# Performance work log

Hardware: AMD Instinct MI355X
Metric: run time of the kernel (lower is better)

## Reference

```python
import jax, jax.numpy as jnp
import numpy as np

EPS = 1e-7  # keras.backend.epsilon()
ROUTINGS = 3


def squash(s, axis=-1):
    # standard capsule squash: ||s||^2/(1+||s||^2) * s/||s||
    n2 = jnp.sum(jnp.square(s), axis=axis, keepdims=True)
    return s * (n2 / (1.0 + n2)) / jnp.sqrt(n2 + EPS)


def setup_inputs() -> dict:
    key = jax.random.key(0)
    k1, k2 = jax.random.split(key)
    B, I, K = 32, 2048, 8          # batch, input capsules, input capsule dim
    J, D = 32, 16                  # output capsules (num_capsules), dim_capsules
    x = jax.random.normal(k1, (B, I, K), dtype=jnp.float32)
    # add_weight with random_normal_initializer(stddev=0.1), shape [J, I, D, K]
    W = 0.1 * jax.random.normal(k2, (J, I, D, K), dtype=jnp.float32)
    return {"x": x, "W": W}


def reference(x, W):
    # u_ji_hat[b,j,i,d] = sum_k W[j,i,d,k] * x[b,i,k]  (the map_fn batched matmul)
    u_hat = jnp.einsum('jidk,bik->bjid', W, x)  # [B, J, I, D]
    B, J, I, D = u_hat.shape
    b = jnp.zeros((B, J, I), dtype=u_hat.dtype)  # routing logits b_ij
    v = None
    for r in range(ROUTINGS):
        c = jax.nn.softmax(b, axis=1)                 # softmax over output capsules J
        s = jnp.einsum('bji,bjid->bjd', c, u_hat)     # weighted sum over input caps i
        v = squash(s, axis=-1)                        # squash over capsule dim (axis=-2 pre-squeeze)
        if r < ROUTINGS - 1:
            # agreement = u_hat^T v : sum over capsule dim d
            b = b + jnp.einsum('bjid,bjd->bji', u_hat, v)
    return v  # [B, J, D] == tf.squeeze(v_j, [2, 4])
```

## Files before the change

kernel.cpp:

```cpp
#include <hip/hip_runtime.h>
#include <hip/hip_fp16.h>


#define ICAP    2048
#define JD      512
#define S_ELEMS 16384
#define EPSQ    1e-7f
#define NBP     256
#define ICH     8

#if defined(__has_builtin) && __has_builtin(__builtin_amdgcn_rcpf)
#define FAST_RCP(x) __builtin_amdgcn_rcpf(x)
#else
#define FAST_RCP(x) (1.0f / (x))
#endif
#if defined(__has_builtin) && __has_builtin(__builtin_amdgcn_rsqf)
#define FAST_RSQ(x) __builtin_amdgcn_rsqf(x)
#else
#define FAST_RSQ(x) rsqrtf(x)
#endif

__global__ __launch_bounds__(256)
void caps_transpose(const float4* __restrict__ Wv, float4* __restrict__ Wt) {
    __shared__ float4 buf[16 * 66];
    const int i = blockIdx.x;
    const int t = threadIdx.x;
#pragma unroll
    for (int q = 0; q < 4; ++q) {
        const int f = q * 256 + t;
        const int jj = f >> 5, c = f & 31;
        buf[(c & 15) * 66 + 2 * jj + (c >> 4)] =
            Wv[(size_t)jj * 65536 + (size_t)i * 32 + c];
    }
    __syncthreads();
    float4* dst = Wt + (size_t)i * 1024;
#pragma unroll
    for (int q = 0; q < 4; ++q) {
        const int o = q * 256 + t;
        dst[o] = buf[(o >> 6) * 66 + (o & 63)];
    }
}

__global__ __launch_bounds__(512, 1)
void caps_pass(const float4* __restrict__ Wt, const float* __restrict__ x,
               const float* __restrict__ vsum, __half* __restrict__ partials) {
    const int tid  = threadIdx.x;
    const int wave = tid >> 6;
    const int lane = tid & 63;
    const int j    = lane & 31;
    const int dh   = lane >> 5;
    const int i0   = blockIdx.x * ICH;

    float vs[4][8], sacc[4][8];
#pragma unroll
    for (int bb = 0; bb < 4; ++bb) {
        const int b = wave + 8 * bb;
        const float* vp = vsum + b * JD + j * 16 + dh * 8;
        float4 a  = *reinterpret_cast<const float4*>(vp);
        float4 bq = *reinterpret_cast<const float4*>(vp + 4);
        vs[bb][0]=a.x; vs[bb][1]=a.y; vs[bb][2]=a.z; vs[bb][3]=a.w;
        vs[bb][4]=bq.x; vs[bb][5]=bq.y; vs[bb][6]=bq.z; vs[bb][7]=bq.w;
#pragma unroll
        for (int r = 0; r < 8; ++r) sacc[bb][r] = 0.f;
    }

    const float4* wp = Wt + (size_t)i0 * 1024 + 2 * j + dh;

#pragma unroll 1
    for (int il = 0; il < ICH; ++il) {
        float4 w4[16];
#pragma unroll
        for (int cc = 0; cc < 16; ++cc)
            w4[cc] = wp[(size_t)il * 1024 + cc * 64];

        const int gi = i0 + il;
#pragma unroll
        for (int bb = 0; bb < 4; ++bb) {
            const int b = wave + 8 * bb;
            const float* xp = x + ((size_t)b * ICAP + gi) * 8;
            const float4 x0 = *reinterpret_cast<const float4*>(xp);
            const float4 x1 = *reinterpret_cast<const float4*>(xp + 4);

            float u[8], tpart = 0.f;
#pragma unroll
            for (int r = 0; r < 8; ++r) {
                const float4 wa = w4[2 * r], wb = w4[2 * r + 1];
                float acc;
                acc = wa.x * x0.x;
                acc = fmaf(wa.y, x0.y, acc);
                acc = fmaf(wa.z, x0.z, acc);
                acc = fmaf(wa.w, x0.w, acc);
                acc = fmaf(wb.x, x1.x, acc);
                acc = fmaf(wb.y, x1.y, acc);
                acc = fmaf(wb.z, x1.z, acc);
                acc = fmaf(wb.w, x1.w, acc);
                u[r] = acc;
                tpart = fmaf(acc, vs[bb][r], tpart);
            }
            const float t = tpart + __shfl_xor(tpart, 32);
            const float e = __expf(t);
            float se = e;
#pragma unroll
            for (int off = 1; off <= 16; off <<= 1)
                se += __shfl_xor(se, off);
            const float c = e * FAST_RCP(se);
#pragma unroll
            for (int r = 0; r < 8; ++r)
                sacc[bb][r] = fmaf(c, u[r], sacc[bb][r]);
        }
    }

    __half* pout = partials + (size_t)blockIdx.x * S_ELEMS;
#pragma unroll
    for (int bb = 0; bb < 4; ++bb) {
        const int b = wave + 8 * bb;
        union { int4 v; __half2 h[4]; } pk;
#pragma unroll
        for (int r = 0; r < 4; ++r)
            pk.h[r] = __floats2half2_rn(sacc[bb][2 * r], sacc[bb][2 * r + 1]);
        *reinterpret_cast<int4*>(pout + b * JD + j * 16 + dh * 8) = pk.v;
    }
}

__global__ __launch_bounds__(1024)
void caps_reduce(const __half* __restrict__ partials, float* __restrict__ vsum,
                 float* __restrict__ out) {
    __shared__ float buf[16][80];
    const int tid = threadIdx.x;
    const int eL  = tid & 63;
    const int sg  = tid >> 6;
    const int e   = blockIdx.x * 64 + eL;

    float s = 0.f;
    const __half* p = partials + (size_t)sg * S_ELEMS + e;
#pragma unroll
    for (int n = 0; n < 16; ++n)
        s += __half2float(p[(size_t)(n * 16) * S_ELEMS]);
    buf[sg][eL] = s;
    __syncthreads();

    if (sg == 0) {
        s = 0.f;
#pragma unroll
        for (int k = 0; k < 16; ++k) s += buf[k][eL];
        float n2 = s * s;
#pragma unroll
        for (int off = 1; off <= 8; off <<= 1)
            n2 += __shfl_xor(n2, off);
        const float scale = n2 * FAST_RCP(1.f + n2) * FAST_RSQ(n2 + EPSQ);
        const float v = s * scale;
        vsum[e] += v;
        if (out) out[e] = v;
    }
}

extern "C" void kernel_launch(void* const* d_in, const int* in_sizes, int n_in,
                              void* d_out, int out_size, void* d_ws, size_t ws_size,
                              hipStream_t stream) {
    const float* x = (const float*)d_in[0];
    const float* W = (const float*)d_in[1];
    float* out = (float*)d_out;

    float4* Wt       = (float4*)d_ws;
    float*  vsum     = (float*)((char*)d_ws + (size_t)ICAP * 1024 * 16);
    __half* partials = (__half*)((char*)vsum + S_ELEMS * sizeof(float));

    hipMemsetAsync(vsum, 0, S_ELEMS * sizeof(float), stream);
    caps_transpose<<<ICAP, 256, 0, stream>>>((const float4*)W, Wt);

    for (int r = 0; r < 3; ++r) {
        caps_pass<<<NBP, 512, 0, stream>>>(Wt, x, vsum, partials);
        caps_reduce<<<S_ELEMS / 64, 1024, 0, stream>>>(
            partials, vsum, (r == 2) ? out : nullptr);
    }
}
```

Measured before the change: 176.3 us.

## Fuse routing into cooperative kernel with fp16 weights and dot2 math

Replaces the transpose plus per-iteration pass/reduce launches with a single cooperative kernel using grid syncs. The first pass converts W and x to fp16 while computing with uniform coupling, skipping the softmax. Later passes read half-size fp16 weights and use packed fdot2. This cuts memory traffic and launch overhead but adds fp16 rounding of inputs and grid-sync costs, with a multi-kernel fallback.

```diff
diff --git a/kernel.cpp b/kernel.cpp
--- a/kernel.cpp
+++ b/kernel.cpp
@@ -1,14 +1,27 @@
 #include <hip/hip_runtime.h>
 #include <hip/hip_fp16.h>
+#include <hip/hip_cooperative_groups.h>
+
+namespace cg = cooperative_groups;
 
 
 #define ICAP    2048
 #define JD      512
 #define S_ELEMS 16384
 #define EPSQ    1e-7f
-#define NBP     256
+#define NBLK    256
 #define ICH     8
 
+typedef _Float16 h2v __attribute__((ext_vector_type(2)));
+union H8 { int4 i4; h2v h[4]; };
+
+#if defined(__has_builtin) && __has_builtin(__builtin_amdgcn_fdot2)
+#define FDOT2(a, b, c) __builtin_amdgcn_fdot2((a), (b), (c), false)
+#else
+__device__ inline float FDOT2(h2v a, h2v b, float c) {
+    return c + (float)a[0] * (float)b[0] + (float)a[1] * (float)b[1];
+}
+#endif
 #if defined(__has_builtin) && __has_builtin(__builtin_amdgcn_rcpf)
 #define FAST_RCP(x) __builtin_amdgcn_rcpf(x)
 #else
@@ -20,71 +33,73 @@
 #define FAST_RSQ(x) rsqrtf(x)
 #endif
 
-__global__ __launch_bounds__(256)
-void caps_transpose(const float4* __restrict__ Wv, float4* __restrict__ Wt) {
-    __shared__ float4 buf[16 * 66];
-    const int i = blockIdx.x;
-    const int t = threadIdx.x;
-#pragma unroll
-    for (int q = 0; q < 4; ++q) {
-        const int f = q * 256 + t;
-        const int jj = f >> 5, c = f & 31;
-        buf[(c & 15) * 66 + 2 * jj + (c >> 4)] =
-            Wv[(size_t)jj * 65536 + (size_t)i * 32 + c];
-    }
-    __syncthreads();
-    float4* dst = Wt + (size_t)i * 1024;
-#pragma unroll
-    for (int q = 0; q < 4; ++q) {
-        const int o = q * 256 + t;
-        dst[o] = buf[(o >> 6) * 66 + (o & 63)];
-    }
-}
-
-__global__ __launch_bounds__(512, 1)
-void caps_pass(const float4* __restrict__ Wt, const float* __restrict__ x,
-               const float* __restrict__ vsum, __half* __restrict__ partials) {
-    const int tid  = threadIdx.x;
-    const int wave = tid >> 6;
-    const int lane = tid & 63;
-    const int j    = lane & 31;
-    const int dh   = lane >> 5;
-    const int i0   = blockIdx.x * ICH;
-
-    float vs[4][8], sacc[4][8];
+__device__ inline void write_partials(int bl, int wave, int j, int dh,
+                                      const float sacc[4][8],
+                                      __half* __restrict__ partials) {
+    __half* pout = partials + (size_t)bl * S_ELEMS;
 #pragma unroll
     for (int bb = 0; bb < 4; ++bb) {
         const int b = wave + 8 * bb;
-        const float* vp = vsum + b * JD + j * 16 + dh * 8;
-        float4 a  = *reinterpret_cast<const float4*>(vp);
-        float4 bq = *reinterpret_cast<const float4*>(vp + 4);
-        vs[bb][0]=a.x; vs[bb][1]=a.y; vs[bb][2]=a.z; vs[bb][3]=a.w;
-        vs[bb][4]=bq.x; vs[bb][5]=bq.y; vs[bb][6]=bq.z; vs[bb][7]=bq.w;
+        union { int4 v; __half2 h[4]; } pk;
+#pragma unroll
+        for (int r = 0; r < 4; ++r)
+            pk.h[r] = __floats2half2_rn(sacc[bb][2 * r], sacc[bb][2 * r + 1]);
+        *reinterpret_cast<int4*>(pout + b * JD + j * 16 + dh * 8) = pk.v;
+    }
+}
+
+__device__ void phase_first(int bl, int tid,
+                            const float4* __restrict__ Wv,
+                            const float* __restrict__ x,
+                            int4* __restrict__ Wt, __half* __restrict__ xh,
+                            __half* __restrict__ partials) {
+    const int wave = tid >> 6, lane = tid & 63;
+    const int j = lane & 31, dh = lane >> 5, m = 2 * j + dh;
+    const int i0 = bl * ICH;
+
+#pragma unroll
+    for (int q = 0; q < 4; ++q) {
+        const int idx = q * 512 + tid;
+        const int b = idx >> 6, r = idx & 63;
+        const size_t xi = (size_t)b * (ICAP * 8) + (size_t)i0 * 8 + r;
+        xh[xi] = __float2half(x[xi]);
+    }
+
+    float sacc[4][8];
+#pragma unroll
+    for (int bb = 0; bb < 4; ++bb)
 #pragma unroll
         for (int r = 0; r < 8; ++r) sacc[bb][r] = 0.f;
-    }
-
-    const float4* wp = Wt + (size_t)i0 * 1024 + 2 * j + dh;
-
-#pragma unroll 1
+
+#pragma unroll 2
     for (int il = 0; il < ICH; ++il) {
-        float4 w4[16];
-#pragma unroll
-        for (int cc = 0; cc < 16; ++cc)
-            w4[cc] = wp[(size_t)il * 1024 + cc * 64];
-
         const int gi = i0 + il;
+        float4 wf[16];
+        const float4* wp = Wv + (size_t)j * 65536 + (size_t)gi * 32 + dh * 16;
+#pragma unroll
+        for (int cc = 0; cc < 16; ++cc) wf[cc] = wp[cc];
+
+        int4* wt = Wt + (size_t)gi * 512 + m;
+#pragma unroll
+        for (int cc = 0; cc < 8; ++cc) {
+            const float4 a = wf[2 * cc], b = wf[2 * cc + 1];
+            H8 h;
+            h.h[0] = h2v{(_Float16)a.x, (_Float16)a.y};
+            h.h[1] = h2v{(_Float16)a.z, (_Float16)a.w};
+            h.h[2] = h2v{(_Float16)b.x, (_Float16)b.y};
+            h.h[3] = h2v{(_Float16)b.z, (_Float16)b.w};
+            wt[cc * 64] = h.i4;
+        }
+
 #pragma unroll
         for (int bb = 0; bb < 4; ++bb) {
             const int b = wave + 8 * bb;
             const float* xp = x + ((size_t)b * ICAP + gi) * 8;
             const float4 x0 = *reinterpret_cast<const float4*>(xp);
             const float4 x1 = *reinterpret_cast<const float4*>(xp + 4);
-
-            float u[8], tpart = 0.f;
 #pragma unroll
             for (int r = 0; r < 8; ++r) {
-                const float4 wa = w4[2 * r], wb = w4[2 * r + 1];
+                const float4 wa = wf[2 * r], wb = wf[2 * r + 1];
                 float acc;
                 acc = wa.x * x0.x;
                 acc = fmaf(wa.y, x0.y, acc);
@@ -94,6 +109,58 @@
                 acc = fmaf(wb.y, x1.y, acc);
                 acc = fmaf(wb.z, x1.z, acc);
                 acc = fmaf(wb.w, x1.w, acc);
+                sacc[bb][r] = fmaf(0.03125f, acc, sacc[bb][r]);
+            }
+        }
+    }
+    write_partials(bl, wave, j, dh, sacc, partials);
+}
+
+__device__ void phase_pass(int bl, int tid,
+                           const int4* __restrict__ Wt,
+                           const int4* __restrict__ xh,
+                           const float* __restrict__ vsum,
+                           __half* __restrict__ partials) {
+    const int wave = tid >> 6, lane = tid & 63;
+    const int j = lane & 31, dh = lane >> 5, m = 2 * j + dh;
+    const int i0 = bl * ICH;
+
+    float vs[4][8], sacc[4][8];
+#pragma unroll
+    for (int bb = 0; bb < 4; ++bb) {
+        const int b = wave + 8 * bb;
+        const float* vp = vsum + b * JD + j * 16 + dh * 8;
+        const float4 a  = *reinterpret_cast<const float4*>(vp);
+        const float4 bq = *reinterpret_cast<const float4*>(vp + 4);
+        vs[bb][0]=a.x; vs[bb][1]=a.y; vs[bb][2]=a.z; vs[bb][3]=a.w;
+        vs[bb][4]=bq.x; vs[bb][5]=bq.y; vs[bb][6]=bq.z; vs[bb][7]=bq.w;
+#pragma unroll
+        for (int r = 0; r < 8; ++r) sacc[bb][r] = 0.f;
+    }
+
+    const int4* wp = Wt + (size_t)i0 * 512 + m;
+
+#pragma unroll 2
+    for (int il = 0; il < ICH; ++il) {
+        H8 w8[8];
+#pragma unroll
+        for (int cc = 0; cc < 8; ++cc)
+            w8[cc].i4 = wp[(size_t)il * 512 + cc * 64];
+
+        const int gi = i0 + il;
+#pragma unroll
+        for (int bb = 0; bb < 4; ++bb) {
+            const int b = wave + 8 * bb;
+            H8 xv;
+            xv.i4 = xh[(size_t)b * ICAP + gi];
+
+            float u[8], tpart = 0.f;
+#pragma unroll
+            for (int r = 0; r < 8; ++r) {
+                float acc = FDOT2(w8[r].h[0], xv.h[0], 0.f);
+                acc = FDOT2(w8[r].h[1], xv.h[1], acc);
+                acc = FDOT2(w8[r].h[2], xv.h[2], acc);
+                acc = FDOT2(w8[r].h[3], xv.h[3], acc);
                 u[r] = acc;
                 tpart = fmaf(acc, vs[bb][r], tpart);
             }
@@ -109,68 +176,105 @@
                 sacc[bb][r] = fmaf(c, u[r], sacc[bb][r]);
         }
     }
-
-    __half* pout = partials + (size_t)blockIdx.x * S_ELEMS;
-#pragma unroll
-    for (int bb = 0; bb < 4; ++bb) {
-        const int b = wave + 8 * bb;
-        union { int4 v; __half2 h[4]; } pk;
-#pragma unroll
-        for (int r = 0; r < 4; ++r)
-            pk.h[r] = __floats2half2_rn(sacc[bb][2 * r], sacc[bb][2 * r + 1]);
-        *reinterpret_cast<int4*>(pout + b * JD + j * 16 + dh * 8) = pk.v;
-    }
-}
-
-__global__ __launch_bounds__(1024)
-void caps_reduce(const __half* __restrict__ partials, float* __restrict__ vsum,
-                 float* __restrict__ out) {
-    __shared__ float buf[16][80];
-    const int tid = threadIdx.x;
-    const int eL  = tid & 63;
-    const int sg  = tid >> 6;
-    const int e   = blockIdx.x * 64 + eL;
-
+    write_partials(bl, wave, j, dh, sacc, partials);
+}
+
+__device__ void phase_reduce(int bl, int tid,
+                             const __half* __restrict__ partials,
+                             float* __restrict__ vsum,
+                             float* __restrict__ out, int ridx) {
+    __shared__ float rbuf[8][72];
+    const int eL = tid & 63, sg = tid >> 6;
+    const int e = bl * 64 + eL;
     float s = 0.f;
     const __half* p = partials + (size_t)sg * S_ELEMS + e;
 #pragma unroll
-    for (int n = 0; n < 16; ++n)
-        s += __half2float(p[(size_t)(n * 16) * S_ELEMS]);
-    buf[sg][eL] = s;
+    for (int n = 0; n < 32; ++n)
+        s += __half2float(p[(size_t)n * 8 * S_ELEMS]);
+    rbuf[sg][eL] = s;
     __syncthreads();
-
-    if (sg == 0) {
+    if (tid < 64) {
         s = 0.f;
 #pragma unroll
-        for (int k = 0; k < 16; ++k) s += buf[k][eL];
+        for (int k = 0; k < 8; ++k) s += rbuf[k][tid];
         float n2 = s * s;
 #pragma unroll
         for (int off = 1; off <= 8; off <<= 1)
             n2 += __shfl_xor(n2, off);
         const float scale = n2 * FAST_RCP(1.f + n2) * FAST_RSQ(n2 + EPSQ);
         const float v = s * scale;
-        vsum[e] += v;
-        if (out) out[e] = v;
-    }
+        const int eo = bl * 64 + tid;
+        if (ridx == 0)      vsum[eo] = v;
+        else if (ridx == 1) vsum[eo] += v;
+        else                out[eo] = v;
+    }
+    __syncthreads();
+}
+
+__global__ __launch_bounds__(512, 2)
+void caps_coop(const float4* __restrict__ Wv, const float* __restrict__ x,
+               int4* __restrict__ Wt, __half* __restrict__ xh,
+               __half* __restrict__ partials, float* __restrict__ vsum,
+               float* __restrict__ out) {
+    cg::grid_group grid = cg::this_grid();
+    const int bl = blockIdx.x, tid = threadIdx.x;
+    phase_first(bl, tid, Wv, x, Wt, xh, partials);
+    grid.sync();
+    phase_reduce(bl, tid, partials, vsum, out, 0);
+    grid.sync();
+    phase_pass(bl, tid, Wt, (const int4*)xh, vsum, partials);
+    grid.sync();
+    phase_reduce(bl, tid, partials, vsum, out, 1);
+    grid.sync();
+    phase_pass(bl, tid, Wt, (const int4*)xh, vsum, partials);
+    grid.sync();
+    phase_reduce(bl, tid, partials, vsum, out, 2);
+}
+
+__global__ __launch_bounds__(512, 2)
+void k_first(const float4* Wv, const float* x, int4* Wt, __half* xh,
+             __half* partials) {
+    phase_first(blockIdx.x, threadIdx.x, Wv, x, Wt, xh, partials);
+}
+__global__ __launch_bounds__(512, 2)
+void k_pass(const int4* Wt, const int4* xh, const float* vsum,
+            __half* partials) {
+    phase_pass(blockIdx.x, threadIdx.x, Wt, xh, vsum, partials);
+}
+__global__ __launch_bounds__(512, 2)
+void k_reduce(const __half* partials, float* vsum, float* out, int ridx) {
+    phase_reduce(blockIdx.x, threadIdx.x, partials, vsum, out, ridx);
 }
 
 extern "C" void kernel_launch(void* const* d_in, const int* in_sizes, int n_in,
                               void* d_out, int out_size, void* d_ws, size_t ws_size,
                               hipStream_t stream) {
-    const float* x = (const float*)d_in[0];
-    const float* W = (const float*)d_in[1];
+    const float*  x  = (const float*)d_in[0];
+    const float4* Wv = (const float4*)d_in[1];
     float* out = (float*)d_out;
 
-    float4* Wt       = (float4*)d_ws;
-    float*  vsum     = (float*)((char*)d_ws + (size_t)ICAP * 1024 * 16);
-    __half* partials = (__half*)((char*)vsum + S_ELEMS * sizeof(float));
-
-    hipMemsetAsync(vsum, 0, S_ELEMS * sizeof(float), stream);
-    caps_transpose<<<ICAP, 256, 0, stream>>>((const float4*)W, Wt);
-
-    for (int r = 0; r < 3; ++r) {
-        caps_pass<<<NBP, 512, 0, stream>>>(Wt, x, vsum, partials);
-        caps_reduce<<<S_ELEMS / 64, 1024, 0, stream>>>(
-            partials, vsum, (r == 2) ? out : nullptr);
-    }
-}
+    int4*   Wt       = (int4*)d_ws;
+    __half* xh       = (__half*)((char*)d_ws + (size_t)ICAP * 512 * 16);
+    __half* partials = (__half*)((char*)xh + (size_t)32 * ICAP * 8 * 2);
+    float*  vsum     = (float*)((char*)partials +
+                                (size_t)NBLK * S_ELEMS * sizeof(__half));
+
+    int occ = 0;
+    bool coop = (hipSuccess == hipOccupancyMaxActiveBlocksPerMultiprocessor(
+                     &occ, reinterpret_cast<const void*>(&caps_coop), 512, 0))
+                && occ >= 1;
+    if (coop) {
+        void* args[] = { (void*)&Wv, (void*)&x, (void*)&Wt, (void*)&xh,
+                         (void*)&partials, (void*)&vsum, (void*)&out };
+        coop = (hipSuccess == hipLaunchCooperativeKernel(
+                    (void*)caps_coop, dim3(NBLK), dim3(512), args, 0, stream));
+    }
+    if (!coop) {
+        k_first<<<NBLK, 512, 0, stream>>>(Wv, x, Wt, xh, partials);
+        k_reduce<<<NBLK, 512, 0, stream>>>(partials, vsum, out, 0);
+        k_pass<<<NBLK, 512, 0, stream>>>(Wt, (const int4*)xh, vsum, partials);
+        k_reduce<<<NBLK, 512, 0, stream>>>(partials, vsum, out, 1);
+        k_pass<<<NBLK, 512, 0, stream>>>(Wt, (const int4*)xh, vsum, partials);
+        k_reduce<<<NBLK, 512, 0, stream>>>(partials, vsum, out, 2);
+    }
+}
```

Result: faster. 164.4 us (-6.7%).
